# Kernel optimization log

Hardware: AMD Instinct MI355X
Metric: run time of the kernel (lower is better)

The kernel has to match this reference:

```python
import jax, jax.numpy as jnp
import numpy as np

N_NODES = 8192
N_EDGES = 65536


def _segment_softmax(scores, seg_ids, num_segments):
    # scores: [E, 1], seg_ids: [E] -> softmax over edges sharing the same dst
    m = jax.ops.segment_max(scores, seg_ids, num_segments=num_segments)  # [N,1]
    e = jnp.exp(scores - m[seg_ids])
    denom = jax.ops.segment_sum(e, seg_ids, num_segments=num_segments)   # [N,1]
    return e / denom[seg_ids]


def setup_inputs() -> dict:
    key = jax.random.key(0)
    ks = jax.random.split(key, 12)
    s = lambda fin: 1.0 / np.sqrt(fin)
    inp = {
        'n_f': jax.random.normal(ks[0], (N_NODES, 1024), jnp.float32),
        'word2vec': jax.random.normal(ks[1], (N_NODES, 300), jnp.float32),
        's_f': jax.random.normal(ks[2], (N_EDGES, 16), jnp.float32),
        'src': jax.random.randint(ks[3], (N_EDGES,), 0, N_NODES),
        'dst': jax.random.randint(ks[4], (N_EDGES,), 0, N_NODES),
        'We': jax.random.normal(ks[5], (2064, 1024), jnp.float32) * s(2064),
        'be': jnp.zeros((1024,), jnp.float32),
        'Wel': jax.random.normal(ks[6], (600, 600), jnp.float32) * s(600),
        'bel': jnp.zeros((600,), jnp.float32),
        'Wa': jax.random.normal(ks[7], (1024, 1), jnp.float32) * s(1024),
        'ba': jnp.zeros((1,), jnp.float32),
        'Wal': jax.random.normal(ks[8], (600, 1), jnp.float32) * s(600),
        'bal': jnp.zeros((1,), jnp.float32),
        'Wn': jax.random.normal(ks[9], (2048, 1024), jnp.float32) * s(2048),
        'bn': jnp.zeros((1024,), jnp.float32),
        'Wnl': jax.random.normal(ks[10], (600, 300), jnp.float32) * s(600),
        'bnl': jnp.zeros((300,), jnp.float32),
    }
    return inp


def reference(n_f, word2vec, s_f, src, dst,
              We, be, Wel, bel, Wa, ba, Wal, bal, Wn, bn, Wnl, bnl):
    # ---- edge apply (H_H_EdgeApplyModule) ----
    src_nf = n_f[src]                                    # [E,1024] gather
    feat = jnp.concatenate([src_nf, s_f, n_f[dst]], axis=1)  # [E,2064]
    e_f = jax.nn.relu(feat @ We + be)                    # [E,1024]
    feat_lang = jnp.concatenate([word2vec[src], word2vec[dst]], axis=1)  # [E,600]
    e_f_lang = jax.nn.relu(feat_lang @ Wel + bel)        # [E,600]

    # ---- edge attention (E_AttentionModule1): scalar score per edge ----
    a_feat = e_f @ Wa + ba                               # [E,1]
    a_feat_lang = e_f_lang @ Wal + bal                   # [E,1]

    # ---- reduce: mailbox softmax over incoming edges per dst node ----
    alpha = _segment_softmax(a_feat, dst, N_NODES)       # [E,1]
    alpha_lang = _segment_softmax(a_feat_lang, dst, N_NODES)
    z_f = jax.ops.segment_sum(alpha * (src_nf + e_f), dst, num_segments=N_NODES)      # [N,1024]
    z_f_lang = jax.ops.segment_sum(alpha_lang * word2vec[src], dst, num_segments=N_NODES)  # [N,300]

    # ---- node apply (H_NodeApplyModule) ----
    new_n_f = jax.nn.relu(jnp.concatenate([n_f, z_f], axis=1) @ Wn + bn)              # [N,1024]
    new_n_f_lang = jax.nn.relu(jnp.concatenate([word2vec, z_f_lang], axis=1) @ Wnl + bnl)  # [N,300]
    return new_n_f, new_n_f_lang
```

## Files before the change

kernel.cpp:

```cpp
#include <hip/hip_runtime.h>
#include <hip/hip_bf16.h>

#define N_NODES 8192
#define N_EDGES 65536
#define OUT0_ELEMS ((size_t)N_NODES * 1024)

using bf16 = __hip_bfloat16;
typedef __attribute__((ext_vector_type(8))) short short8;
typedef __attribute__((ext_vector_type(4))) float f32x4;

__device__ __forceinline__ float b2f(bf16 x) { return __bfloat162float(x); }
__device__ __forceinline__ bf16 f2b(float x) { return __float2bfloat16(x); }
__device__ __forceinline__ unsigned short bbits(float x)
{
  union { bf16 h; unsigned short u; } v; v.h = f2b(x); return v.u;
}
__device__ __forceinline__ unsigned pack2(float a, float b)
{
  return (unsigned)bbits(a) | ((unsigned)bbits(b) << 16);
}
__device__ __forceinline__ float4 ld4b(const bf16* p)
{
  uint2 u = *(const uint2*)p;
  float4 r;
  r.x = __uint_as_float(u.x << 16);
  r.y = __uint_as_float(u.x & 0xffff0000u);
  r.z = __uint_as_float(u.y << 16);
  r.w = __uint_as_float(u.y & 0xffff0000u);
  return r;
}
__device__ __forceinline__ void st4b(bf16* p, float a, float b, float c, float d)
{
  uint2 v; v.x = pack2(a, b); v.y = pack2(c, d);
  *(uint2*)p = v;
}

__global__ void GNN_27650999451833_kernel() {}

__global__ void gnn6_zero(int* __restrict__ p, int n)
{
  int i = blockIdx.x * blockDim.x + threadIdx.x;
  if (i < n) p[i] = 0;
}

__global__ __launch_bounds__(256)
void gnn7_cvt(const float* __restrict__ src, bf16* __restrict__ dst, int n8)
{
  int i = blockIdx.x * blockDim.x + threadIdx.x;
  if (i < n8) {
    float4 a = ((const float4*)src)[2 * i];
    float4 b = ((const float4*)src)[2 * i + 1];
    uint4 p;
    p.x = pack2(a.x, a.y); p.y = pack2(a.z, a.w);
    p.z = pack2(b.x, b.y); p.w = pack2(b.z, b.w);
    ((uint4*)dst)[i] = p;
  }
}

__global__ __launch_bounds__(256)
void gnn8_pad_w2v(const float* __restrict__ src, bf16* __restrict__ dst)
{
  int idx = blockIdx.x * blockDim.x + threadIdx.x;
  if (idx >= N_NODES * 80) return;
  int r = idx / 80, c0 = (idx % 80) * 4;
  float v[4];
#pragma unroll
  for (int j = 0; j < 4; ++j) {
    int c = c0 + j;
    v[j] = (c < 300) ? src[(size_t)r * 300 + c] : 0.f;
  }
  uint2 p; p.x = pack2(v[0], v[1]); p.y = pack2(v[2], v[3]);
  *(uint2*)(dst + (size_t)r * 320 + c0) = p;
}

__global__ __launch_bounds__(256)
void gnn12_sf_pad(const float* __restrict__ s_f, bf16* __restrict__ sf_pad)
{
  int e = blockIdx.x * 256 + threadIdx.x;
  if (e >= N_EDGES) return;
  const float4* sp = (const float4*)(s_f + (size_t)e * 16);
  float4 s0 = sp[0], s1 = sp[1], s2 = sp[2], s3 = sp[3];
  uint4 lo, hi;
  lo.x = pack2(s0.x, s0.y); lo.y = pack2(s0.z, s0.w);
  lo.z = pack2(s1.x, s1.y); lo.w = pack2(s1.z, s1.w);
  hi.x = pack2(s2.x, s2.y); hi.y = pack2(s2.z, s2.w);
  hi.z = pack2(s3.x, s3.y); hi.w = pack2(s3.z, s3.w);
  uint4* dp = (uint4*)(sf_pad + (size_t)e * 32);
  dp[0] = lo; dp[1] = hi;
  dp[2] = (uint4){0, 0, 0, 0}; dp[3] = (uint4){0, 0, 0, 0};
}

__global__ __launch_bounds__(256)
void gnn12_t_Wetail(const float* __restrict__ We, bf16* __restrict__ BT)
{
  int c = blockIdx.x * 256 + threadIdx.x;
  if (c >= 1024) return;
  bf16* row = BT + (size_t)c * 32;
#pragma unroll
  for (int k = 0; k < 16; ++k)
    row[k] = f2b(We[(size_t)(1024 + k) * 1024 + c]);
#pragma unroll
  for (int k = 16; k < 32; ++k) row[k] = f2b(0.f);
}

__global__ __launch_bounds__(256)
void gnn10_t_We(const float* __restrict__ src, bf16* __restrict__ dst)
{
  __shared__ float tile[32][33];
  const int kb = blockIdx.x * 32, nb = blockIdx.y * 32;
  const int tx = threadIdx.x & 31, ty = threadIdx.x >> 5;
  const int n = nb + tx;
#pragma unroll
  for (int i = ty; i < 32; i += 8)
    tile[i][tx] = (n < 1024)
        ? src[(size_t)(kb + i) * 1024 + n]
        : src[(size_t)(1040 + kb + i) * 1024 + (n - 1024)];
  __syncthreads();
#pragma unroll
  for (int i = ty; i < 32; i += 8)
    dst[(size_t)(nb + i) * 1024 + kb + tx] = f2b(tile[tx][i]);
}

__global__ __launch_bounds__(256)
void gnn10_t_Wn(const float* __restrict__ src, bf16* __restrict__ dst)
{
  __shared__ float tile[32][33];
  const int kb = blockIdx.x * 32, nb = blockIdx.y * 32;
  const int tx = threadIdx.x & 31, ty = threadIdx.x >> 5;
#pragma unroll
  for (int i = ty; i < 32; i += 8)
    tile[i][tx] = src[(size_t)(kb + i) * 1024 + nb + tx];
  __syncthreads();
#pragma unroll
  for (int i = ty; i < 32; i += 8)
    dst[(size_t)(nb + i) * 2048 + kb + tx] = f2b(tile[tx][i]);
}

__global__ __launch_bounds__(256)
void gnn10_t_Wel(const float* __restrict__ src, bf16* __restrict__ dst)
{
  __shared__ float tile[32][33];
  const int kb = blockIdx.x * 32, nb = blockIdx.y * 32;
  const int tx = threadIdx.x & 31, ty = threadIdx.x >> 5;
  const int n = nb + tx;
#pragma unroll
  for (int i = ty; i < 32; i += 8) {
    int k = kb + i;
    float v = 0.f;
    if (k < 300) {
      if (n < 600)       v = src[(size_t)k * 600 + n];
      else if (n < 1200) v = src[(size_t)(300 + k) * 600 + (n - 600)];
    }
    tile[i][tx] = v;
  }
  __syncthreads();
#pragma unroll
  for (int i = ty; i < 32; i += 8)
    dst[(size_t)(nb + i) * 320 + kb + tx] = f2b(tile[tx][i]);
}

__global__ __launch_bounds__(256)
void gnn10_t_Wnl(const float* __restrict__ src, bf16* __restrict__ dst)
{
  __shared__ float tile[32][33];
  const int kb = blockIdx.x * 32, nb = blockIdx.y * 32;
  const int tx = threadIdx.x & 31, ty = threadIdx.x >> 5;
  const int n = nb + tx;
#pragma unroll
  for (int i = ty; i < 32; i += 8) {
    int k = kb + i;
    int kr = (k < 300) ? k : ((k >= 320 && k < 620) ? (k - 20) : -1);
    tile[i][tx] = (kr >= 0 && n < 300) ? src[(size_t)kr * 300 + n] : 0.f;
  }
  __syncthreads();
#pragma unroll
  for (int i = ty; i < 32; i += 8)
    dst[(size_t)(nb + i) * 640 + kb + tx] = f2b(tile[tx][i]);
}

__global__ __launch_bounds__(256)
void gnn10_mm_P(const bf16* __restrict__ A, const bf16* __restrict__ BT,
                bf16* __restrict__ P, const float* __restrict__ be)
{
  __shared__ short As[128 * 40];
  __shared__ short Bs[128 * 40];
  const int t = threadIdx.x;
  const int col0 = blockIdx.x * 128, row0 = blockIdx.y * 128;
  const int lane = t & 63, w = t >> 6, m16 = lane & 15, q = lane >> 4;
  const int wr = w >> 1, wc = w & 1;

  f32x4 acc[4][4];
#pragma unroll
  for (int mi = 0; mi < 4; ++mi)
#pragma unroll
    for (int ni = 0; ni < 4; ++ni) acc[mi][ni] = (f32x4){0.f, 0.f, 0.f, 0.f};

  const int ar = t >> 1, ah = (t & 1) * 16;
  const bf16* aptr = A + (size_t)(row0 + ar) * 1024 + ah;
  const bf16* bptr = BT + (size_t)(col0 + ar) * 1024 + ah;

  uint4 a0 = *(const uint4*)(aptr);
  uint4 a1 = *(const uint4*)(aptr + 8);
  uint4 b0 = *(const uint4*)(bptr);
  uint4 b1 = *(const uint4*)(bptr + 8);

  for (int k0 = 0; k0 < 1024; k0 += 32) {
    if (k0) __syncthreads();
    *(uint4*)&As[ar * 40 + ah] = a0;
    *(uint4*)&As[ar * 40 + ah + 8] = a1;
    *(uint4*)&Bs[ar * 40 + ah] = b0;
    *(uint4*)&Bs[ar * 40 + ah + 8] = b1;
    __syncthreads();
    if (k0 + 32 < 1024) {
      a0 = *(const uint4*)(aptr + k0 + 32);
      a1 = *(const uint4*)(aptr + k0 + 40);
      b0 = *(const uint4*)(bptr + k0 + 32);
      b1 = *(const uint4*)(bptr + k0 + 40);
    }
    short8 af[4];
#pragma unroll
    for (int mi = 0; mi < 4; ++mi)
      af[mi] = *(const short8*)&As[(wr * 64 + mi * 16 + m16) * 40 + 8 * q];
#pragma unroll
    for (int ni = 0; ni < 4; ++ni) {
      short8 bfv = *(const short8*)&Bs[(wc * 64 + ni * 16 + m16) * 40 + 8 * q];
#pragma unroll
      for (int mi = 0; mi < 4; ++mi)
        acc[mi][ni] =
            __builtin_amdgcn_mfma_f32_16x16x32_bf16(af[mi], bfv, acc[mi][ni], 0, 0, 0);
    }
  }
#pragma unroll
  for (int mi = 0; mi < 4; ++mi)
#pragma unroll
    for (int ni = 0; ni < 4; ++ni) {
      int c = col0 + wc * 64 + ni * 16 + m16;
      float bias = (be != nullptr && c >= 1024) ? be[c - 1024] : 0.f;
#pragma unroll
      for (int r = 0; r < 4; ++r)
        P[(size_t)(row0 + wr * 64 + mi * 16 + 4 * q + r) * 2048 + c] =
            f2b(acc[mi][ni][r] + bias);
    }
}

__global__ __launch_bounds__(256)
void gnn10_mm_out_n(const bf16* __restrict__ A0, const bf16* __restrict__ A1,
                    const bf16* __restrict__ BT, const float* __restrict__ bn,
                    float* __restrict__ out)
{
  __shared__ short As[128 * 40];
  __shared__ short Bs[128 * 40];
  const int t = threadIdx.x;
  const int col0 = blockIdx.x * 128, row0 = blockIdx.y * 128;
  const int lane = t & 63, w = t >> 6, m16 = lane & 15, q = lane >> 4;
  const int wr = w >> 1, wc = w & 1;

  f32x4 acc[4][4];
#pragma unroll
  for (int mi = 0; mi < 4; ++mi)
#pragma unroll
    for (int ni = 0; ni < 4; ++ni) acc[mi][ni] = (f32x4){0.f, 0.f, 0.f, 0.f};

  const int ar = t >> 1, ah = (t & 1) * 16;
  const bf16* ap0 = A0 + (size_t)(row0 + ar) * 1024 + ah;
  const bf16* ap1 = A1 + (size_t)(row0 + ar) * 1024 + ah;
  const bf16* bptr = BT + (size_t)(col0 + ar) * 2048 + ah;

  uint4 a0 = *(const uint4*)(ap0);
  uint4 a1 = *(const uint4*)(ap0 + 8);
  uint4 b0 = *(const uint4*)(bptr);
  uint4 b1 = *(const uint4*)(bptr + 8);

  for (int k0 = 0; k0 < 2048; k0 += 32) {
    if (k0) __syncthreads();
    *(uint4*)&As[ar * 40 + ah] = a0;
    *(uint4*)&As[ar * 40 + ah + 8] = a1;
    *(uint4*)&Bs[ar * 40 + ah] = b0;
    *(uint4*)&Bs[ar * 40 + ah + 8] = b1;
    __syncthreads();
    if (k0 + 32 < 2048) {
      int kn = k0 + 32;
      const bf16* ap = (kn < 1024) ? (ap0 + kn) : (ap1 + (kn - 1024));
      a0 = *(const uint4*)(ap);
      a1 = *(const uint4*)(ap + 8);
      b0 = *(const uint4*)(bptr + kn);
      b1 = *(const uint4*)(bptr + kn + 8);
    }
    short8 af[4];
#pragma unroll
    for (int mi = 0; mi < 4; ++mi)
      af[mi] = *(const short8*)&As[(wr * 64 + mi * 16 + m16) * 40 + 8 * q];
#pragma unroll
    for (int ni = 0; ni < 4; ++ni) {
      short8 bfv = *(const short8*)&Bs[(wc * 64 + ni * 16 + m16) * 40 + 8 * q];
#pragma unroll
      for (int mi = 0; mi < 4; ++mi)
        acc[mi][ni] =
            __builtin_amdgcn_mfma_f32_16x16x32_bf16(af[mi], bfv, acc[mi][ni], 0, 0, 0);
    }
  }
#pragma unroll
  for (int mi = 0; mi < 4; ++mi)
#pragma unroll
    for (int ni = 0; ni < 4; ++ni) {
      int c = col0 + wc * 64 + ni * 16 + m16;
      float bias = bn[c];
#pragma unroll
      for (int r = 0; r < 4; ++r) {
        float v = acc[mi][ni][r] + bias;
        out[(size_t)(row0 + wr * 64 + mi * 16 + 4 * q + r) * 1024 + c] =
            fmaxf(v, 0.f);
      }
    }
}

__global__ __launch_bounds__(256)
void gnn10_mm_Q(const bf16* __restrict__ A, const bf16* __restrict__ BT,
                bf16* __restrict__ Q, const float* __restrict__ bel)
{
  __shared__ short As[128 * 40];
  __shared__ short Bs[128 * 40];
  const int t = threadIdx.x;
  const int col0 = blockIdx.x * 128, row0 = blockIdx.y * 128;
  const int lane = t & 63, w = t >> 6, m16 = lane & 15, q = lane >> 4;
  const int wr = w >> 1, wc = w & 1;

  f32x4 acc[4][4];
#pragma unroll
  for (int mi = 0; mi < 4; ++mi)
#pragma unroll
    for (int ni = 0; ni < 4; ++ni) acc[mi][ni] = (f32x4){0.f, 0.f, 0.f, 0.f};

  const int ar = t >> 1, ah = (t & 1) * 16;
  const bf16* aptr = A + (size_t)(row0 + ar) * 320 + ah;
  const bf16* bptr = BT + (size_t)(col0 + ar) * 320 + ah;

  uint4 a0 = *(const uint4*)(aptr);
  uint4 a1 = *(const uint4*)(aptr + 8);
  uint4 b0 = *(const uint4*)(bptr);
  uint4 b1 = *(const uint4*)(bptr + 8);

  for (int k0 = 0; k0 < 320; k0 += 32) {
    if (k0) __syncthreads();
    *(uint4*)&As[ar * 40 + ah] = a0;
    *(uint4*)&As[ar * 40 + ah + 8] = a1;
    *(uint4*)&Bs[ar * 40 + ah] = b0;
    *(uint4*)&Bs[ar * 40 + ah + 8] = b1;
    __syncthreads();
    if (k0 + 32 < 320) {
      a0 = *(const uint4*)(aptr + k0 + 32);
      a1 = *(const uint4*)(aptr + k0 + 40);
      b0 = *(const uint4*)(bptr + k0 + 32);
      b1 = *(const uint4*)(bptr + k0 + 40);
    }
    short8 af[4];
#pragma unroll
    for (int mi = 0; mi < 4; ++mi)
      af[mi] = *(const short8*)&As[(wr * 64 + mi * 16 + m16) * 40 + 8 * q];
#pragma unroll
    for (int ni = 0; ni < 4; ++ni) {
      short8 bfv = *(const short8*)&Bs[(wc * 64 + ni * 16 + m16) * 40 + 8 * q];
#pragma unroll
      for (int mi = 0; mi < 4; ++mi)
        acc[mi][ni] =
            __builtin_amdgcn_mfma_f32_16x16x32_bf16(af[mi], bfv, acc[mi][ni], 0, 0, 0);
    }
  }
#pragma unroll
  for (int mi = 0; mi < 4; ++mi)
#pragma unroll
    for (int ni = 0; ni < 4; ++ni) {
      int c = col0 + wc * 64 + ni * 16 + m16;
      float bias = (bel != nullptr && c >= 600 && c < 1200) ? bel[c - 600] : 0.f;
#pragma unroll
      for (int r = 0; r < 4; ++r)
        Q[(size_t)(row0 + wr * 64 + mi * 16 + 4 * q + r) * 1280 + c] =
            f2b(acc[mi][ni][r] + bias);
    }
}

__global__ __launch_bounds__(256)
void gnn10_mm_out_l(const bf16* __restrict__ A0, const bf16* __restrict__ A1,
                    const bf16* __restrict__ BT, const float* __restrict__ bnl,
                    float* __restrict__ out2)
{
  __shared__ short As[128 * 40];
  __shared__ short Bs[128 * 40];
  const int t = threadIdx.x;
  const int col0 = blockIdx.x * 128, row0 = blockIdx.y * 128;
  const int lane = t & 63, w = t >> 6, m16 = lane & 15, q = lane >> 4;
  const int wr = w >> 1, wc = w & 1;

  f32x4 acc[4][4];
#pragma unroll
  for (int mi = 0; mi < 4; ++mi)
#pragma unroll
    for (int ni = 0; ni < 4; ++ni) acc[mi][ni] = (f32x4){0.f, 0.f, 0.f, 0.f};

  const int ar = t >> 1, ah = (t & 1) * 16;
  const bf16* ap0 = A0 + (size_t)(row0 + ar) * 320 + ah;
  const bf16* ap1 = A1 + (size_t)(row0 + ar) * 320 + ah;
  const bf16* bptr = BT + (size_t)(col0 + ar) * 640 + ah;

  uint4 a0 = *(const uint4*)(ap0);
  uint4 a1 = *(const uint4*)(ap0 + 8);
  uint4 b0 = *(const uint4*)(bptr);
  uint4 b1 = *(const uint4*)(bptr + 8);

  for (int k0 = 0; k0 < 640; k0 += 32) {
    if (k0) __syncthreads();
    *(uint4*)&As[ar * 40 + ah] = a0;
    *(uint4*)&As[ar * 40 + ah + 8] = a1;
    *(uint4*)&Bs[ar * 40 + ah] = b0;
    *(uint4*)&Bs[ar * 40 + ah + 8] = b1;
    __syncthreads();
    if (k0 + 32 < 640) {
      int kn = k0 + 32;
      const bf16* ap = (kn < 320) ? (ap0 + kn) : (ap1 + (kn - 320));
      a0 = *(const uint4*)(ap);
      a1 = *(const uint4*)(ap + 8);
      b0 = *(const uint4*)(bptr + kn);
      b1 = *(const uint4*)(bptr + kn + 8);
    }
    short8 af[4];
#pragma unroll
    for (int mi = 0; mi < 4; ++mi)
      af[mi] = *(const short8*)&As[(wr * 64 + mi * 16 + m16) * 40 + 8 * q];
#pragma unroll
    for (int ni = 0; ni < 4; ++ni) {
      short8 bfv = *(const short8*)&Bs[(wc * 64 + ni * 16 + m16) * 40 + 8 * q];
#pragma unroll
      for (int mi = 0; mi < 4; ++mi)
        acc[mi][ni] =
            __builtin_amdgcn_mfma_f32_16x16x32_bf16(af[mi], bfv, acc[mi][ni], 0, 0, 0);
    }
  }
#pragma unroll
  for (int mi = 0; mi < 4; ++mi)
#pragma unroll
    for (int ni = 0; ni < 4; ++ni) {
      int c = col0 + wc * 64 + ni * 16 + m16;
      if (c < 300) {
        float bias = bnl[c];
#pragma unroll
        for (int r = 0; r < 4; ++r) {
          float v = acc[mi][ni][r] + bias;
          out2[(size_t)(row0 + wr * 64 + mi * 16 + 4 * q + r) * 300 + c] =
              fmaxf(v, 0.f);
        }
      }
    }
}

__global__ __launch_bounds__(256)
void gnn12_mm_S(const bf16* __restrict__ A, const bf16* __restrict__ BT,
                bf16* __restrict__ S)
{
  __shared__ short As[128 * 40];
  __shared__ short Bs[128 * 40];
  const int t = threadIdx.x;
  const int col0 = blockIdx.x * 128, row0 = blockIdx.y * 128;
  const int lane = t & 63, w = t >> 6, m16 = lane & 15, q = lane >> 4;
  const int wr = w >> 1, wc = w & 1;

  const int ar = t >> 1, ah = (t & 1) * 16;
  *(uint4*)&As[ar * 40 + ah]     = *(const uint4*)(A + (size_t)(row0 + ar) * 32 + ah);
  *(uint4*)&As[ar * 40 + ah + 8] = *(const uint4*)(A + (size_t)(row0 + ar) * 32 + ah + 8);
  *(uint4*)&Bs[ar * 40 + ah]     = *(const uint4*)(BT + (size_t)(col0 + ar) * 32 + ah);
  *(uint4*)&Bs[ar * 40 + ah + 8] = *(const uint4*)(BT + (size_t)(col0 + ar) * 32 + ah + 8);
  __syncthreads();

  f32x4 acc[4][4];
#pragma unroll
  for (int mi = 0; mi < 4; ++mi)
#pragma unroll
    for (int ni = 0; ni < 4; ++ni) acc[mi][ni] = (f32x4){0.f, 0.f, 0.f, 0.f};

  short8 af[4];
#pragma unroll
  for (int mi = 0; mi < 4; ++mi)
    af[mi] = *(const short8*)&As[(wr * 64 + mi * 16 + m16) * 40 + 8 * q];
#pragma unroll
  for (int ni = 0; ni < 4; ++ni) {
    short8 bfv = *(const short8*)&Bs[(wc * 64 + ni * 16 + m16) * 40 + 8 * q];
#pragma unroll
    for (int mi = 0; mi < 4; ++mi)
      acc[mi][ni] =
          __builtin_amdgcn_mfma_f32_16x16x32_bf16(af[mi], bfv, acc[mi][ni], 0, 0, 0);
  }

#pragma unroll
  for (int mi = 0; mi < 4; ++mi)
#pragma unroll
    for (int ni = 0; ni < 4; ++ni) {
      int c = col0 + wc * 64 + ni * 16 + m16;
#pragma unroll
      for (int r = 0; r < 4; ++r)
        S[(size_t)(row0 + wr * 64 + mi * 16 + 4 * q + r) * 1024 + c] =
            f2b(acc[mi][ni][r]);
    }
}

__global__ __launch_bounds__(256)
void gnn12_edge_score(const int* __restrict__ src, const int* __restrict__ dst,
                      const bf16* __restrict__ S, const float* __restrict__ Wa,
                      const float* __restrict__ ba, const float* __restrict__ Wal,
                      const float* __restrict__ bal, const bf16* __restrict__ P,
                      const bf16* __restrict__ Q, float* __restrict__ af,
                      float* __restrict__ afl)
{
  const int t = threadIdx.x;
  const int lane = t & 63, w = t >> 6;
  const int c0 = 4 * t;
  const int e0 = blockIdx.x * 8;

  float4 wav = *(const float4*)(Wa + c0);
  const bool lact = (t < 150);
  float4 walv = {0, 0, 0, 0};
  if (lact) walv = *(const float4*)(Wal + c0);

  int ss[8], dd[8];
  {
    int4 a = *(const int4*)(src + e0);
    int4 b = *(const int4*)(src + e0 + 4);
    ss[0] = a.x; ss[1] = a.y; ss[2] = a.z; ss[3] = a.w;
    ss[4] = b.x; ss[5] = b.y; ss[6] = b.z; ss[7] = b.w;
    int4 c = *(const int4*)(dst + e0);
    int4 d = *(const int4*)(dst + e0 + 4);
    dd[0] = c.x; dd[1] = c.y; dd[2] = c.z; dd[3] = c.w;
    dd[4] = d.x; dd[5] = d.y; dd[6] = d.z; dd[7] = d.w;
  }

  float pf[8], pl[8];

#pragma unroll
  for (int i = 0; i < 8; ++i) {
    const int e = e0 + i;
    float4 sv = ld4b(S + (size_t)e * 1024 + c0);
    float4 p1 = ld4b(P + (size_t)ss[i] * 2048 + c0);
    float4 p2 = ld4b(P + (size_t)dd[i] * 2048 + 1024 + c0);
    float acc = 0.f;
    acc = fmaf(fmaxf(p1.x + p2.x + sv.x, 0.f), wav.x, acc);
    acc = fmaf(fmaxf(p1.y + p2.y + sv.y, 0.f), wav.y, acc);
    acc = fmaf(fmaxf(p1.z + p2.z + sv.z, 0.f), wav.z, acc);
    acc = fmaf(fmaxf(p1.w + p2.w + sv.w, 0.f), wav.w, acc);
    pf[i] = acc;

    float accl = 0.f;
    if (lact) {
      float4 q1 = ld4b(Q + (size_t)ss[i] * 1280 + c0);
      float4 q2 = ld4b(Q + (size_t)dd[i] * 1280 + 600 + c0);
      accl = fmaf(fmaxf(q1.x + q2.x, 0.f), walv.x, accl);
      accl = fmaf(fmaxf(q1.y + q2.y, 0.f), walv.y, accl);
      accl = fmaf(fmaxf(q1.z + q2.z, 0.f), walv.z, accl);
      accl = fmaf(fmaxf(q1.w + q2.w, 0.f), walv.w, accl);
    }
    pl[i] = accl;
  }

  __shared__ float shf[8][4], shl[8][4];
#pragma unroll
  for (int i = 0; i < 8; ++i) {
#pragma unroll
    for (int o = 32; o > 0; o >>= 1) {
      pf[i] += __shfl_down(pf[i], o, 64);
      pl[i] += __shfl_down(pl[i], o, 64);
    }
  }
  if (lane == 0) {
#pragma unroll
    for (int i = 0; i < 8; ++i) { shf[i][w] = pf[i]; shl[i][w] = pl[i]; }
  }
  __syncthreads();
  if (t < 8)
    af[e0 + t] = shf[t][0] + shf[t][1] + shf[t][2] + shf[t][3] + ba[0];
  if (t >= 64 && t < 72) {
    const int i = t & 7;
    afl[e0 + i] = shl[i][0] + shl[i][1] + shl[i][2] + shl[i][3] + bal[0];
  }
}

__global__ __launch_bounds__(256)
void gnn11_edge_score(const int* __restrict__ src, const int* __restrict__ dst,
                      const float* __restrict__ s_f, const float* __restrict__ We,
                      const float* __restrict__ be, const float* __restrict__ Wa,
                      const float* __restrict__ ba, const float* __restrict__ bel,
                      const float* __restrict__ Wal, const float* __restrict__ bal,
                      const bf16* __restrict__ P, const bf16* __restrict__ Q,
                      float* __restrict__ af, float* __restrict__ afl)
{
  const int t = threadIdx.x;
  const int lane = t & 63, w = t >> 6;
  const int c0 = 4 * t;
  const int e0 = blockIdx.x * 8;

  float wef[16][4];
#pragma unroll
  for (int k = 0; k < 16; ++k) {
    float4 v = *(const float4*)(We + (size_t)(1024 + k) * 1024 + c0);
    wef[k][0] = v.x; wef[k][1] = v.y; wef[k][2] = v.z; wef[k][3] = v.w;
  }
  float4 bev = *(const float4*)(be + c0);
  float4 wav = *(const float4*)(Wa + c0);
  const bool lact = (t < 150);
  float4 belv = {0, 0, 0, 0}, walv = {0, 0, 0, 0};
  if (lact) { belv = *(const float4*)(bel + c0); walv = *(const float4*)(Wal + c0); }

  int ss[8], dd[8];
  {
    int4 a = *(const int4*)(src + e0);
    int4 b = *(const int4*)(src + e0 + 4);
    ss[0] = a.x; ss[1] = a.y; ss[2] = a.z; ss[3] = a.w;
    ss[4] = b.x; ss[5] = b.y; ss[6] = b.z; ss[7] = b.w;
    int4 c = *(const int4*)(dst + e0);
    int4 d = *(const int4*)(dst + e0 + 4);
    dd[0] = c.x; dd[1] = c.y; dd[2] = c.z; dd[3] = c.w;
    dd[4] = d.x; dd[5] = d.y; dd[6] = d.z; dd[7] = d.w;
  }

  float pf[8], pl[8];

#pragma unroll
  for (int i = 0; i < 8; ++i) {
    const int e = e0 + i;
    float sfv[16];
    {
      const float4* sp = (const float4*)(s_f + (size_t)e * 16);
      float4 s0 = sp[0], s1 = sp[1], s2 = sp[2], s3 = sp[3];
      sfv[0] = s0.x; sfv[1] = s0.y; sfv[2] = s0.z; sfv[3] = s0.w;
      sfv[4] = s1.x; sfv[5] = s1.y; sfv[6] = s1.z; sfv[7] = s1.w;
      sfv[8] = s2.x; sfv[9] = s2.y; sfv[10] = s2.z; sfv[11] = s2.w;
      sfv[12] = s3.x; sfv[13] = s3.y; sfv[14] = s3.z; sfv[15] = s3.w;
    }
    float4 p1 = ld4b(P + (size_t)ss[i] * 2048 + c0);
    float4 p2 = ld4b(P + (size_t)dd[i] * 2048 + 1024 + c0);
    float pv[4] = {p1.x + p2.x + bev.x, p1.y + p2.y + bev.y,
                   p1.z + p2.z + bev.z, p1.w + p2.w + bev.w};
    float acc = 0.f;
#pragma unroll
    for (int j = 0; j < 4; ++j) {
      float v = pv[j];
#pragma unroll
      for (int k = 0; k < 16; ++k) v = fmaf(sfv[k], wef[k][j], v);
      acc = fmaf(fmaxf(v, 0.f), (&wav.x)[j], acc);
    }
    pf[i] = acc;

    float accl = 0.f;
    if (lact) {
      float4 q1 = ld4b(Q + (size_t)ss[i] * 1280 + c0);
      float4 q2 = ld4b(Q + (size_t)dd[i] * 1280 + 600 + c0);
      float qv[4] = {q1.x + q2.x + belv.x, q1.y + q2.y + belv.y,
                     q1.z + q2.z + belv.z, q1.w + q2.w + belv.w};
#pragma unroll
      for (int j = 0; j < 4; ++j)
        accl = fmaf(fmaxf(qv[j], 0.f), (&walv.x)[j], accl);
    }
    pl[i] = accl;
  }

  __shared__ float shf[8][4], shl[8][4];
#pragma unroll
  for (int i = 0; i < 8; ++i) {
#pragma unroll
    for (int o = 32; o > 0; o >>= 1) {
      pf[i] += __shfl_down(pf[i], o, 64);
      pl[i] += __shfl_down(pl[i], o, 64);
    }
  }
  if (lane == 0) {
#pragma unroll
    for (int i = 0; i < 8; ++i) { shf[i][w] = pf[i]; shl[i][w] = pl[i]; }
  }
  __syncthreads();
  if (t < 8)
    af[e0 + t] = shf[t][0] + shf[t][1] + shf[t][2] + shf[t][3] + ba[0];
  if (t >= 64 && t < 72) {
    const int i = t & 7;
    afl[e0 + i] = shl[i][0] + shl[i][1] + shl[i][2] + shl[i][3] + bal[0];
  }
}

__global__ void gnn6_count(const int* __restrict__ dst, int* __restrict__ cnt)
{
  int e = blockIdx.x * blockDim.x + threadIdx.x;
  if (e < N_EDGES) atomicAdd(&cnt[dst[e]], 1);
}

__global__ __launch_bounds__(1024)
void gnn6_scan(const int* __restrict__ cnt, int* __restrict__ off, int* __restrict__ cur)
{
  __shared__ int sh[1024];
  const int t = threadIdx.x;
  int local[8]; int sum = 0;
#pragma unroll
  for (int i = 0; i < 8; ++i) { int v = cnt[t * 8 + i]; local[i] = sum; sum += v; }
  sh[t] = sum;
  __syncthreads();
  for (int d = 1; d < 1024; d <<= 1) {
    int v = (t >= d) ? sh[t - d] : 0;
    __syncthreads();
    sh[t] += v;
    __syncthreads();
  }
  int basev = (t > 0) ? sh[t - 1] : 0;
#pragma unroll
  for (int i = 0; i < 8; ++i) { int o = basev + local[i]; off[t * 8 + i] = o; cur[t * 8 + i] = o; }
  if (t == 1023) off[8192] = sh[1023];
}

__global__ void gnn6_fill(const int* __restrict__ dst, int* __restrict__ cur,
                          int* __restrict__ elist)
{
  int e = blockIdx.x * blockDim.x + threadIdx.x;
  if (e < N_EDGES) { int p = atomicAdd(&cur[dst[e]], 1); elist[p] = e; }
}

__global__ __launch_bounds__(256)
void gnn6_alpha(const int* __restrict__ off, const int* __restrict__ elist,
                float* __restrict__ af, float* __restrict__ afl)
{
  const int n = blockIdx.x * 256 + threadIdx.x;
  if (n >= N_NODES) return;
  const int base = off[n];
  const int deg = off[n + 1] - base;
  float m = -1e30f, ml = -1e30f;
  for (int i = 0; i < deg; ++i) {
    int e = elist[base + i];
    m = fmaxf(m, af[e]);
    ml = fmaxf(ml, afl[e]);
  }
  float den = 0.f, denl = 0.f;
  for (int i = 0; i < deg; ++i) {
    int e = elist[base + i];
    den += expf(af[e] - m);
    denl += expf(afl[e] - ml);
  }
  float inv = (den > 0.f) ? 1.f / den : 0.f;
  float invl = (denl > 0.f) ? 1.f / denl : 0.f;
  for (int i = 0; i < deg; ++i) {
    int e = elist[base + i];
    af[e] = expf(af[e] - m) * inv;
    afl[e] = expf(afl[e] - ml) * invl;
  }
}

__global__ __launch_bounds__(256)
void gnn12_node_z(const int* __restrict__ off, const int* __restrict__ elist,
                  const int* __restrict__ src, const float* __restrict__ af,
                  const float* __restrict__ afl, const bf16* __restrict__ nf_bf,
                  const bf16* __restrict__ w2v_pad, const bf16* __restrict__ S,
                  const bf16* __restrict__ P, bf16* __restrict__ zf,
                  bf16* __restrict__ zfl_pad)
{
  const int node = blockIdx.x;
  const int t = threadIdx.x;
  const int c0 = 4 * t;
  const int base = off[node];
  const int deg = off[node + 1] - base;

  float4 p2v = ld4b(P + (size_t)node * 2048 + 1024 + c0);
  const float p2[4] = {p2v.x, p2v.y, p2v.z, p2v.w};

  float acc[4] = {0.f, 0.f, 0.f, 0.f};
  float accl[4] = {0.f, 0.f, 0.f, 0.f};
  const bool lact = (t < 75);

  for (int i = 0; i < deg; ++i) {
    const int e = elist[base + i];
    const int s = src[e];
    const float wgt = af[e];
    const float wl = afl[e];

    float4 sv = ld4b(S + (size_t)e * 1024 + c0);
    float4 p1 = ld4b(P + (size_t)s * 2048 + c0);
    float4 nf4 = ld4b(nf_bf + (size_t)s * 1024 + c0);
    const float p1a[4] = {p1.x, p1.y, p1.z, p1.w};
    const float sva[4] = {sv.x, sv.y, sv.z, sv.w};
    const float nfa[4] = {nf4.x, nf4.y, nf4.z, nf4.w};
#pragma unroll
    for (int j = 0; j < 4; ++j) {
      float ef = fmaxf(p1a[j] + p2[j] + sva[j], 0.f);
      acc[j] = fmaf(wgt, nfa[j] + ef, acc[j]);
    }
    if (lact) {
      float4 wv = ld4b(w2v_pad + (size_t)s * 320 + c0);
      accl[0] = fmaf(wl, wv.x, accl[0]);
      accl[1] = fmaf(wl, wv.y, accl[1]);
      accl[2] = fmaf(wl, wv.z, accl[2]);
      accl[3] = fmaf(wl, wv.w, accl[3]);
    }
  }
  st4b(zf + (size_t)node * 1024 + c0, acc[0], acc[1], acc[2], acc[3]);
  if (lact)
    st4b(zfl_pad + (size_t)node * 320 + c0, accl[0], accl[1], accl[2], accl[3]);
  else if (t < 80)
    st4b(zfl_pad + (size_t)node * 320 + c0, 0.f, 0.f, 0.f, 0.f);
}

__global__ __launch_bounds__(256)
void gnn9_node_z(const int* __restrict__ off, const int* __restrict__ elist,
                 const int* __restrict__ src, const float* __restrict__ af,
                 const float* __restrict__ afl, const bf16* __restrict__ nf_bf,
                 const bf16* __restrict__ w2v_pad, const float* __restrict__ s_f,
                 const float* __restrict__ We, const float* __restrict__ be,
                 const bf16* __restrict__ P, bf16* __restrict__ zf,
                 bf16* __restrict__ zfl_pad)
{
  const int node = blockIdx.x;
  const int t = threadIdx.x;
  const int c0 = 4 * t;
  const int base = off[node];
  const int deg = off[node + 1] - base;

  float wef[16][4];
#pragma unroll
  for (int k = 0; k < 16; ++k) {
    float4 v = *(const float4*)(We + (size_t)(1024 + k) * 1024 + c0);
    wef[k][0] = v.x; wef[k][1] = v.y; wef[k][2] = v.z; wef[k][3] = v.w;
  }
  float4 p2v = ld4b(P + (size_t)node * 2048 + 1024 + c0);
  float4 bev = *(const float4*)(be + c0);
  const float p2[4] = {p2v.x + bev.x, p2v.y + bev.y, p2v.z + bev.z, p2v.w + bev.w};

  float acc[4] = {0.f, 0.f, 0.f, 0.f};
  float accl[4] = {0.f, 0.f, 0.f, 0.f};
  const bool lact = (t < 75);

  for (int i = 0; i < deg; ++i) {
    const int e = elist[base + i];
    const int s = src[e];
    const float wgt = af[e];
    const float wl = afl[e];

    float sfv[16];
    {
      const float4* sp = (const float4*)(s_f + (size_t)e * 16);
      float4 s0 = sp[0], s1 = sp[1], s2 = sp[2], s3 = sp[3];
      sfv[0] = s0.x; sfv[1] = s0.y; sfv[2] = s0.z; sfv[3] = s0.w;
      sfv[4] = s1.x; sfv[5] = s1.y; sfv[6] = s1.z; sfv[7] = s1.w;
      sfv[8] = s2.x; sfv[9] = s2.y; sfv[10] = s2.z; sfv[11] = s2.w;
      sfv[12] = s3.x; sfv[13] = s3.y; sfv[14] = s3.z; sfv[15] = s3.w;
    }

    float4 p1 = ld4b(P + (size_t)s * 2048 + c0);
    float4 nf4 = ld4b(nf_bf + (size_t)s * 1024 + c0);
    const float p1a[4] = {p1.x, p1.y, p1.z, p1.w};
    const float nfa[4] = {nf4.x, nf4.y, nf4.z, nf4.w};
#pragma unroll
    for (int j = 0; j < 4; ++j) {
      float ef = p1a[j] + p2[j];
#pragma unroll
      for (int k = 0; k < 16; ++k) ef = fmaf(sfv[k], wef[k][j], ef);
      ef = fmaxf(ef, 0.f);
      acc[j] = fmaf(wgt, nfa[j] + ef, acc[j]);
    }
    if (lact) {
      float4 wv = ld4b(w2v_pad + (size_t)s * 320 + c0);
      accl[0] = fmaf(wl, wv.x, accl[0]);
      accl[1] = fmaf(wl, wv.y, accl[1]);
      accl[2] = fmaf(wl, wv.z, accl[2]);
      accl[3] = fmaf(wl, wv.w, accl[3]);
    }
  }
  st4b(zf + (size_t)node * 1024 + c0, acc[0], acc[1], acc[2], acc[3]);
  if (lact)
    st4b(zfl_pad + (size_t)node * 320 + c0, accl[0], accl[1], accl[2], accl[3]);
  else if (t < 80)
    st4b(zfl_pad + (size_t)node * 320 + c0, 0.f, 0.f, 0.f, 0.f);
}

extern "C" void kernel_launch(void* const* d_in, const int* in_sizes, int n_in,
                              void* d_out, int out_size, void* d_ws, size_t ws_size,
                              hipStream_t stream)
{
  (void)hipGetLastError();
  if (n_in != 17) { (void)hipMemsetAsync(d_out, 0x41, 4096, stream); return; }

  const float* n_f = (const float*)d_in[0];
  const float* w2v = (const float*)d_in[1];
  const float* s_f = (const float*)d_in[2];
  const int*   src = (const int*)d_in[3];
  const int*   dst = (const int*)d_in[4];
  const float* We  = (const float*)d_in[5];
  const float* be  = (const float*)d_in[6];
  const float* Wel = (const float*)d_in[7];
  const float* bel = (const float*)d_in[8];
  const float* Wa  = (const float*)d_in[9];
  const float* ba  = (const float*)d_in[10];
  const float* Wal = (const float*)d_in[11];
  const float* bal = (const float*)d_in[12];
  const float* Wn  = (const float*)d_in[13];
  const float* bn  = (const float*)d_in[14];
  const float* Wnl = (const float*)d_in[15];
  const float* bnl = (const float*)d_in[16];
  float* out  = (float*)d_out;
  float* out2 = out + OUT0_ELEMS;

  char* ws = (char*)d_ws;
  size_t o = 0;
  auto alloc = [&](size_t bytes) -> void* {
    void* p = ws + o; o += bytes; o = (o + 255) & ~(size_t)255; return p;
  };
  bf16* P        = (bf16*)alloc((size_t)N_NODES * 2048 * 2);
  bf16* Q        = (bf16*)alloc((size_t)N_NODES * 1280 * 2);
  bf16* zf       = (bf16*)alloc((size_t)N_NODES * 1024 * 2);
  bf16* zfl_pad  = (bf16*)alloc((size_t)N_NODES * 320 * 2);
  bf16* nf_bf    = (bf16*)alloc((size_t)N_NODES * 1024 * 2);
  bf16* w2v_pad  = (bf16*)alloc((size_t)N_NODES * 320 * 2);
  bf16* WeT      = (bf16*)alloc((size_t)2048 * 1024 * 2);
  bf16* WnT      = (bf16*)alloc((size_t)1024 * 2048 * 2);
  bf16* WelT     = (bf16*)alloc((size_t)1280 * 320 * 2);
  bf16* WnlT     = (bf16*)alloc((size_t)384 * 640 * 2);
  float* af      = (float*)alloc((size_t)N_EDGES * 4);
  float* afl     = (float*)alloc((size_t)N_EDGES * 4);
  int* cnt       = (int*)alloc((size_t)N_NODES * 4);
  int* offs      = (int*)alloc((size_t)(N_NODES + 1) * 4);
  int* cur       = (int*)alloc((size_t)N_NODES * 4);
  int* elist     = (int*)alloc((size_t)N_EDGES * 4);
  size_t base_end = o;
  if (base_end > ws_size) { (void)hipMemsetAsync(d_out, 0x42, 4096, stream); return; }

  bf16* sf_pad  = (bf16*)alloc((size_t)N_EDGES * 32 * 2);
  bf16* WeTtail = (bf16*)alloc((size_t)1024 * 32 * 2);
  bf16* S       = (bf16*)alloc((size_t)N_EDGES * 1024 * 2);
  const bool useS = (o <= ws_size);

  gnn6_zero<<<N_NODES / 256, 256, 0, stream>>>(cnt, N_NODES);
  gnn7_cvt<<<(N_NODES * 1024 / 8 + 255) / 256, 256, 0, stream>>>(n_f, nf_bf,
                                                                 N_NODES * 1024 / 8);
  gnn8_pad_w2v<<<(N_NODES * 80 + 255) / 256, 256, 0, stream>>>(w2v, w2v_pad);
  { dim3 g(32, 64); gnn10_t_We<<<g, 256, 0, stream>>>(We, WeT); }
  { dim3 g(64, 32); gnn10_t_Wn<<<g, 256, 0, stream>>>(Wn, WnT); }
  { dim3 g(10, 40); gnn10_t_Wel<<<g, 256, 0, stream>>>(Wel, WelT); }
  { dim3 g(20, 12); gnn10_t_Wnl<<<g, 256, 0, stream>>>(Wnl, WnlT); }
  if (useS) {
    gnn12_sf_pad<<<N_EDGES / 256, 256, 0, stream>>>(s_f, sf_pad);
    gnn12_t_Wetail<<<4, 256, 0, stream>>>(We, WeTtail);
  }

  {
    dim3 g(2048 / 128, N_NODES / 128);
    gnn10_mm_P<<<g, 256, 0, stream>>>(nf_bf, WeT, P, useS ? be : nullptr);
  }
  {
    dim3 g(1280 / 128, N_NODES / 128);
    gnn10_mm_Q<<<g, 256, 0, stream>>>(w2v_pad, WelT, Q, useS ? bel : nullptr);
  }
  if (useS) {
    dim3 g(1024 / 128, N_EDGES / 128);
    gnn12_mm_S<<<g, 256, 0, stream>>>(sf_pad, WeTtail, S);
  }

  if (useS) {
    gnn12_edge_score<<<N_EDGES / 8, 256, 0, stream>>>(src, dst, S, Wa, ba, Wal,
                                                      bal, P, Q, af, afl);
  } else {
    gnn11_edge_score<<<N_EDGES / 8, 256, 0, stream>>>(src, dst, s_f, We, be, Wa,
                                                      ba, bel, Wal, bal, P, Q,
                                                      af, afl);
  }

  gnn6_count<<<N_EDGES / 256, 256, 0, stream>>>(dst, cnt);
  gnn6_scan<<<1, 1024, 0, stream>>>(cnt, offs, cur);
  gnn6_fill<<<N_EDGES / 256, 256, 0, stream>>>(dst, cur, elist);
  gnn6_alpha<<<N_NODES / 256, 256, 0, stream>>>(offs, elist, af, afl);

  if (useS) {
    gnn12_node_z<<<N_NODES, 256, 0, stream>>>(offs, elist, src, af, afl, nf_bf,
                                              w2v_pad, S, P, zf, zfl_pad);
  } else {
    gnn9_node_z<<<N_NODES, 256, 0, stream>>>(offs, elist, src, af, afl, nf_bf,
                                             w2v_pad, s_f, We, be, P, zf, zfl_pad);
  }

  {
    dim3 g(1024 / 128, N_NODES / 128);
    gnn10_mm_out_n<<<g, 256, 0, stream>>>(nf_bf, zf, WnT, bn, out);
  }
  {
    dim3 g(384 / 128, N_NODES / 128);
    gnn10_mm_out_l<<<g, 256, 0, stream>>>(w2v_pad, zfl_pad, WnlT, bnl, out2);
  }

  if (hipGetLastError() != hipSuccess) (void)hipMemsetAsync(d_out, 0x44, 4096, stream);
}
```

Baseline: 515.6 us.

## Fuse s_f edge matmul into edge score kernel via shared-memory staging

Merges the small per-edge s_f @ We_tail MFMA matmul into the edge score kernel. Each block computes a 16-edge by 1024-column S tile into LDS and writes it to global for the later node_z kernel. The score pass then reads S from LDS instead of re-reading it from global memory. This drops one kernel launch and one global read of S, at the cost of about 33KB of LDS per block (lower occupancy) and an extra barrier per 8-edge batch.

```diff
diff --git a/kernel.cpp b/kernel.cpp
--- a/kernel.cpp
+++ b/kernel.cpp
@@ -19,15 +19,19 @@
 {
   return (unsigned)bbits(a) | ((unsigned)bbits(b) << 16);
 }
-__device__ __forceinline__ float4 ld4b(const bf16* p)
-{
-  uint2 u = *(const uint2*)p;
+__device__ __forceinline__ float4 cvt2x(uint2 u)
+{
   float4 r;
   r.x = __uint_as_float(u.x << 16);
   r.y = __uint_as_float(u.x & 0xffff0000u);
   r.z = __uint_as_float(u.y << 16);
   r.w = __uint_as_float(u.y & 0xffff0000u);
   return r;
+}
+__device__ __forceinline__ float4 ld4b(const bf16* p)
+{
+  uint2 u = *(const uint2*)p;
+  return cvt2x(u);
 }
 __device__ __forceinline__ void st4b(bf16* p, float a, float b, float c, float d)
 {
@@ -452,131 +456,113 @@
     }
 }
 
-__global__ __launch_bounds__(256)
-void gnn12_mm_S(const bf16* __restrict__ A, const bf16* __restrict__ BT,
-                bf16* __restrict__ S)
-{
-  __shared__ short As[128 * 40];
-  __shared__ short Bs[128 * 40];
+#define SLD_STRIDE 1032
+__global__ __launch_bounds__(256)
+void gnn13_mm_S_score(const bf16* __restrict__ sfp, const bf16* __restrict__ WeTtail,
+                      const int* __restrict__ src, const int* __restrict__ dst,
+                      const float* __restrict__ Wa, const float* __restrict__ ba,
+                      const float* __restrict__ Wal, const float* __restrict__ bal,
+                      const bf16* __restrict__ P, const bf16* __restrict__ Q,
+                      bf16* __restrict__ S, float* __restrict__ af,
+                      float* __restrict__ afl)
+{
+  __shared__ short Sld[16 * SLD_STRIDE];
+  __shared__ float shf[8][4], shl[8][4];
   const int t = threadIdx.x;
-  const int col0 = blockIdx.x * 128, row0 = blockIdx.y * 128;
   const int lane = t & 63, w = t >> 6, m16 = lane & 15, q = lane >> 4;
-  const int wr = w >> 1, wc = w & 1;
-
-  const int ar = t >> 1, ah = (t & 1) * 16;
-  *(uint4*)&As[ar * 40 + ah]     = *(const uint4*)(A + (size_t)(row0 + ar) * 32 + ah);
-  *(uint4*)&As[ar * 40 + ah + 8] = *(const uint4*)(A + (size_t)(row0 + ar) * 32 + ah + 8);
-  *(uint4*)&Bs[ar * 40 + ah]     = *(const uint4*)(BT + (size_t)(col0 + ar) * 32 + ah);
-  *(uint4*)&Bs[ar * 40 + ah + 8] = *(const uint4*)(BT + (size_t)(col0 + ar) * 32 + ah + 8);
+  const int e0 = blockIdx.x * 16;
+
+  short8 afr = *(const short8*)(sfp + (size_t)(e0 + m16) * 32 + 8 * q);
+  const int cb = w * 256;
+#pragma unroll
+  for (int ni = 0; ni < 16; ++ni) {
+    const int col = cb + ni * 16 + m16;
+    short8 bfr = *(const short8*)(WeTtail + (size_t)col * 32 + 8 * q);
+    f32x4 acc = __builtin_amdgcn_mfma_f32_16x16x32_bf16(
+        afr, bfr, (f32x4){0.f, 0.f, 0.f, 0.f}, 0, 0, 0);
+#pragma unroll
+    for (int r = 0; r < 4; ++r)
+      Sld[(4 * q + r) * SLD_STRIDE + col] = (short)bbits(acc[r]);
+  }
   __syncthreads();
 
-  f32x4 acc[4][4];
-#pragma unroll
-  for (int mi = 0; mi < 4; ++mi)
-#pragma unroll
-    for (int ni = 0; ni < 4; ++ni) acc[mi][ni] = (f32x4){0.f, 0.f, 0.f, 0.f};
-
-  short8 af[4];
-#pragma unroll
-  for (int mi = 0; mi < 4; ++mi)
-    af[mi] = *(const short8*)&As[(wr * 64 + mi * 16 + m16) * 40 + 8 * q];
-#pragma unroll
-  for (int ni = 0; ni < 4; ++ni) {
-    short8 bfv = *(const short8*)&Bs[(wc * 64 + ni * 16 + m16) * 40 + 8 * q];
-#pragma unroll
-    for (int mi = 0; mi < 4; ++mi)
-      acc[mi][ni] =
-          __builtin_amdgcn_mfma_f32_16x16x32_bf16(af[mi], bfv, acc[mi][ni], 0, 0, 0);
-  }
-
-#pragma unroll
-  for (int mi = 0; mi < 4; ++mi)
-#pragma unroll
-    for (int ni = 0; ni < 4; ++ni) {
-      int c = col0 + wc * 64 + ni * 16 + m16;
-#pragma unroll
-      for (int r = 0; r < 4; ++r)
-        S[(size_t)(row0 + wr * 64 + mi * 16 + 4 * q + r) * 1024 + c] =
-            f2b(acc[mi][ni][r]);
-    }
-}
-
-__global__ __launch_bounds__(256)
-void gnn12_edge_score(const int* __restrict__ src, const int* __restrict__ dst,
-                      const bf16* __restrict__ S, const float* __restrict__ Wa,
-                      const float* __restrict__ ba, const float* __restrict__ Wal,
-                      const float* __restrict__ bal, const bf16* __restrict__ P,
-                      const bf16* __restrict__ Q, float* __restrict__ af,
-                      float* __restrict__ afl)
-{
-  const int t = threadIdx.x;
-  const int lane = t & 63, w = t >> 6;
+  {
+    const int row = t >> 4, cseg = (t & 15) * 64;
+#pragma unroll
+    for (int j = 0; j < 8; ++j) {
+      uint4 v = *(const uint4*)&Sld[row * SLD_STRIDE + cseg + 8 * j];
+      *(uint4*)(S + (size_t)(e0 + row) * 1024 + cseg + 8 * j) = v;
+    }
+  }
+
   const int c0 = 4 * t;
-  const int e0 = blockIdx.x * 8;
-
   float4 wav = *(const float4*)(Wa + c0);
   const bool lact = (t < 150);
   float4 walv = {0, 0, 0, 0};
   if (lact) walv = *(const float4*)(Wal + c0);
-
-  int ss[8], dd[8];
-  {
-    int4 a = *(const int4*)(src + e0);
-    int4 b = *(const int4*)(src + e0 + 4);
-    ss[0] = a.x; ss[1] = a.y; ss[2] = a.z; ss[3] = a.w;
-    ss[4] = b.x; ss[5] = b.y; ss[6] = b.z; ss[7] = b.w;
-    int4 c = *(const int4*)(dst + e0);
-    int4 d = *(const int4*)(dst + e0 + 4);
-    dd[0] = c.x; dd[1] = c.y; dd[2] = c.z; dd[3] = c.w;
-    dd[4] = d.x; dd[5] = d.y; dd[6] = d.z; dd[7] = d.w;
-  }
-
-  float pf[8], pl[8];
-
-#pragma unroll
-  for (int i = 0; i < 8; ++i) {
-    const int e = e0 + i;
-    float4 sv = ld4b(S + (size_t)e * 1024 + c0);
-    float4 p1 = ld4b(P + (size_t)ss[i] * 2048 + c0);
-    float4 p2 = ld4b(P + (size_t)dd[i] * 2048 + 1024 + c0);
-    float acc = 0.f;
-    acc = fmaf(fmaxf(p1.x + p2.x + sv.x, 0.f), wav.x, acc);
-    acc = fmaf(fmaxf(p1.y + p2.y + sv.y, 0.f), wav.y, acc);
-    acc = fmaf(fmaxf(p1.z + p2.z + sv.z, 0.f), wav.z, acc);
-    acc = fmaf(fmaxf(p1.w + p2.w + sv.w, 0.f), wav.w, acc);
-    pf[i] = acc;
-
-    float accl = 0.f;
-    if (lact) {
-      float4 q1 = ld4b(Q + (size_t)ss[i] * 1280 + c0);
-      float4 q2 = ld4b(Q + (size_t)dd[i] * 1280 + 600 + c0);
-      accl = fmaf(fmaxf(q1.x + q2.x, 0.f), walv.x, accl);
-      accl = fmaf(fmaxf(q1.y + q2.y, 0.f), walv.y, accl);
-      accl = fmaf(fmaxf(q1.z + q2.z, 0.f), walv.z, accl);
-      accl = fmaf(fmaxf(q1.w + q2.w, 0.f), walv.w, accl);
-    }
-    pl[i] = accl;
-  }
-
-  __shared__ float shf[8][4], shl[8][4];
-#pragma unroll
-  for (int i = 0; i < 8; ++i) {
-#pragma unroll
-    for (int o = 32; o > 0; o >>= 1) {
-      pf[i] += __shfl_down(pf[i], o, 64);
-      pl[i] += __shfl_down(pl[i], o, 64);
-    }
-  }
-  if (lane == 0) {
-#pragma unroll
-    for (int i = 0; i < 8; ++i) { shf[i][w] = pf[i]; shl[i][w] = pl[i]; }
-  }
-  __syncthreads();
-  if (t < 8)
-    af[e0 + t] = shf[t][0] + shf[t][1] + shf[t][2] + shf[t][3] + ba[0];
-  if (t >= 64 && t < 72) {
-    const int i = t & 7;
-    afl[e0 + i] = shl[i][0] + shl[i][1] + shl[i][2] + shl[i][3] + bal[0];
+  const float ba0 = ba[0], bal0 = bal[0];
+
+#pragma unroll 1
+  for (int bb = 0; bb < 2; ++bb) {
+    const int eb = 8 * bb;
+    int ss[8], dd[8];
+    {
+      int4 a4 = *(const int4*)(src + e0 + eb);
+      int4 b4 = *(const int4*)(src + e0 + eb + 4);
+      ss[0] = a4.x; ss[1] = a4.y; ss[2] = a4.z; ss[3] = a4.w;
+      ss[4] = b4.x; ss[5] = b4.y; ss[6] = b4.z; ss[7] = b4.w;
+      int4 c4 = *(const int4*)(dst + e0 + eb);
+      int4 d4 = *(const int4*)(dst + e0 + eb + 4);
+      dd[0] = c4.x; dd[1] = c4.y; dd[2] = c4.z; dd[3] = c4.w;
+      dd[4] = d4.x; dd[5] = d4.y; dd[6] = d4.z; dd[7] = d4.w;
+    }
+
+    float pf[8], pl[8];
+#pragma unroll
+    for (int i = 0; i < 8; ++i) {
+      uint2 us = *(const uint2*)&Sld[(eb + i) * SLD_STRIDE + c0];
+      float4 sv = cvt2x(us);
+      float4 p1 = ld4b(P + (size_t)ss[i] * 2048 + c0);
+      float4 p2 = ld4b(P + (size_t)dd[i] * 2048 + 1024 + c0);
+      float acc = 0.f;
+      acc = fmaf(fmaxf(p1.x + p2.x + sv.x, 0.f), wav.x, acc);
+      acc = fmaf(fmaxf(p1.y + p2.y + sv.y, 0.f), wav.y, acc);
+      acc = fmaf(fmaxf(p1.z + p2.z + sv.z, 0.f), wav.z, acc);
+      acc = fmaf(fmaxf(p1.w + p2.w + sv.w, 0.f), wav.w, acc);
+      pf[i] = acc;
+
+      float accl = 0.f;
+      if (lact) {
+        float4 q1 = ld4b(Q + (size_t)ss[i] * 1280 + c0);
+        float4 q2 = ld4b(Q + (size_t)dd[i] * 1280 + 600 + c0);
+        accl = fmaf(fmaxf(q1.x + q2.x, 0.f), walv.x, accl);
+        accl = fmaf(fmaxf(q1.y + q2.y, 0.f), walv.y, accl);
+        accl = fmaf(fmaxf(q1.z + q2.z, 0.f), walv.z, accl);
+        accl = fmaf(fmaxf(q1.w + q2.w, 0.f), walv.w, accl);
+      }
+      pl[i] = accl;
+    }
+
+#pragma unroll
+    for (int i = 0; i < 8; ++i) {
+#pragma unroll
+      for (int o = 32; o > 0; o >>= 1) {
+        pf[i] += __shfl_down(pf[i], o, 64);
+        pl[i] += __shfl_down(pl[i], o, 64);
+      }
+    }
+    if (lane == 0) {
+#pragma unroll
+      for (int i = 0; i < 8; ++i) { shf[i][w] = pf[i]; shl[i][w] = pl[i]; }
+    }
+    __syncthreads();
+    if (t < 8)
+      af[e0 + eb + t] = shf[t][0] + shf[t][1] + shf[t][2] + shf[t][3] + ba0;
+    if (t >= 64 && t < 72) {
+      const int i = t & 7;
+      afl[e0 + eb + i] = shl[i][0] + shl[i][1] + shl[i][2] + shl[i][3] + bal0;
+    }
+    __syncthreads();
   }
 }
 
@@ -947,14 +933,10 @@
     dim3 g(1280 / 128, N_NODES / 128);
     gnn10_mm_Q<<<g, 256, 0, stream>>>(w2v_pad, WelT, Q, useS ? bel : nullptr);
   }
+
   if (useS) {
-    dim3 g(1024 / 128, N_EDGES / 128);
-    gnn12_mm_S<<<g, 256, 0, stream>>>(sf_pad, WeTtail, S);
-  }
-
-  if (useS) {
-    gnn12_edge_score<<<N_EDGES / 8, 256, 0, stream>>>(src, dst, S, Wa, ba, Wal,
-                                                      bal, P, Q, af, afl);
+    gnn13_mm_S_score<<<N_EDGES / 16, 256, 0, stream>>>(
+        sf_pad, WeTtail, src, dst, Wa, ba, Wal, bal, P, Q, S, af, afl);
   } else {
     gnn11_edge_score<<<N_EDGES / 8, 256, 0, stream>>>(src, dst, s_f, We, be, Wa,
                                                       ba, bel, Wal, bal, P, Q,
```

Result: no change. 517.6 us (+0.4%).
